# Optimization experiments

Hardware: AMD Instinct MI355X
Metric: run time of the kernel (lower is better)

Reference implementation:

```python
import jax, jax.numpy as jnp
import numpy as np

D_MODEL = 768
N_HEADS = 12
D_K = D_MODEL // N_HEADS
BATCH = 1
SEQ = 4096


def setup_inputs() -> dict:
    key = jax.random.key(0)
    kx, kq, kk, kv, ko = jax.random.split(key, 5)
    s = 1.0 / np.sqrt(D_MODEL)
    return {
        "x": jax.random.normal(kx, (BATCH, SEQ, D_MODEL), dtype=jnp.float32),
        "wq": jax.random.normal(kq, (D_MODEL, D_MODEL), dtype=jnp.float32) * s,
        "wk": jax.random.normal(kk, (D_MODEL, D_MODEL), dtype=jnp.float32) * s,
        "wv": jax.random.normal(kv, (D_MODEL, D_MODEL), dtype=jnp.float32) * s,
        "wo": jax.random.normal(ko, (D_MODEL, D_MODEL), dtype=jnp.float32) * s,
    }


def reference(x, wq, wk, wv, wo):
    B, S, D = x.shape
    H, dk = N_HEADS, D_K
    # nn.Linear(x) = x @ W.T ; reshape to [B,H,S,dk]
    def proj(w):
        return (x @ w.T).reshape(B, S, H, dk).transpose(0, 2, 1, 3)
    q, k, v = proj(wq), proj(wk), proj(wv)
    scores = jnp.einsum('bhqd,bhkd->bhqk', q, k) / np.sqrt(dk).astype(np.float32)
    attn = jax.nn.softmax(scores, axis=-1)
    out = jnp.einsum('bhqk,bhkd->bhqd', attn, v)
    out = out.transpose(0, 2, 1, 3).reshape(B, S, D)
    return out @ wo.T
```

## Files before the change

### kernel.cpp

```cpp
#include <hip/hip_runtime.h>
#include <stdint.h>

#define SEQ 4096
#define DMODEL 768
#define NHEADS 12
#define DKH 64

typedef __attribute__((ext_vector_type(8))) short short8;
typedef __attribute__((ext_vector_type(4))) float floatx4;
typedef __attribute__((ext_vector_type(16))) float floatx16;

__device__ __forceinline__ unsigned short f2bf(float f) {
    unsigned int u = __float_as_uint(f);
    u += 0x7fffu + ((u >> 16) & 1u);
    return (unsigned short)(u >> 16);
}

__device__ __forceinline__ float exp2fast(float x) {
    return __builtin_amdgcn_exp2f(x);
}

__device__ __forceinline__ unsigned int cvt_pk_bf16(float lo, float hi) {
    unsigned int r;
    asm("v_cvt_pk_bf16_f32 %0, %1, %2" : "=v"(r) : "v"(lo), "v"(hi));
    return r;
}

__device__ __forceinline__ int swz(int row, int colb) {
    return colb ^ ((row & 7) << 4);
}

__device__ __forceinline__ void async_copy16(void* lds, const void* g) {
    __builtin_amdgcn_global_load_lds(
        (const __attribute__((address_space(1))) void*)g,
        (__attribute__((address_space(3))) void*)lds,
        16, 0, 0);
}

__global__ __launch_bounds__(256) void castk(const float* __restrict__ src,
                                             unsigned short* __restrict__ dst,
                                             int n4) {
    int i = blockIdx.x * 256 + threadIdx.x;
    if (i >= n4) return;
    float4 v = ((const float4*)src)[i];
    ushort4 o;
    o.x = f2bf(v.x); o.y = f2bf(v.y); o.z = f2bf(v.z); o.w = f2bf(v.w);
    ((ushort4*)dst)[i] = o;
}

__global__ __launch_bounds__(256) void castw(const float* __restrict__ w0,
                                             const float* __restrict__ w1,
                                             const float* __restrict__ w2,
                                             const float* __restrict__ w3,
                                             unsigned short* __restrict__ dst) {
    int b = blockIdx.x;
    int wsel = b / 576;
    int i = (b % 576) * 256 + threadIdx.x;
    const float* src = (wsel == 0) ? w0 : (wsel == 1) ? w1 : (wsel == 2) ? w2 : w3;
    float4 v = ((const float4*)src)[i];
    ushort4 o;
    o.x = f2bf(v.x); o.y = f2bf(v.y); o.z = f2bf(v.z); o.w = f2bf(v.w);
    ((ushort4*)(dst + (size_t)wsel * 589824))[i] = o;
}

#define STAGE_G(bsel, kb)                                                              \
    do {                                                                               \
        char* As_ = smem + (bsel) * 24576;                                             \
        _Pragma("unroll") for (int ii = 0; ii < 4; ii++) {                             \
            int o = ii * 4096 + t * 16;                                                \
            int row = o >> 7, colb = o & 127;                                          \
            async_copy16(As_ + ii * 4096 + wid * 1024,                                 \
                         (const char*)A + ((size_t)(rowBase + row) * DMODEL + (kb)) * 2 \
                             + swz(row, colb));                                        \
        }                                                                              \
        _Pragma("unroll") for (int ii = 0; ii < 2; ii++) {                             \
            int o = ii * 4096 + t * 16;                                                \
            int row = o >> 7, colb = o & 127;                                          \
            async_copy16(As_ + 16384 + ii * 4096 + wid * 1024,                         \
                         (const char*)B + ((size_t)(colBase + row) * DMODEL + (kb)) * 2 \
                             + swz(row, colb));                                        \
        }                                                                              \
    } while (0)

#define GEMM_COMPUTE(As, Bs)                                                           \
    do {                                                                               \
        short8 a_[4][2], b_[2][2];                                                     \
        _Pragma("unroll") for (int m = 0; m < 4; m++)                                  \
            _Pragma("unroll") for (int kk = 0; kk < 2; kk++) {                         \
                int row = wr * 64 + m * 16 + lr;                                       \
                int colb = kk * 64 + lg * 16;                                          \
                a_[m][kk] = *(const short8*)((As) + row * 128 + swz(row, colb));       \
            }                                                                          \
        _Pragma("unroll") for (int n = 0; n < 2; n++)                                  \
            _Pragma("unroll") for (int kk = 0; kk < 2; kk++) {                         \
                int row = wc * 32 + n * 16 + lr;                                       \
                int colb = kk * 64 + lg * 16;                                          \
                b_[n][kk] = *(const short8*)((Bs) + row * 128 + swz(row, colb));       \
            }                                                                          \
        _Pragma("unroll") for (int m = 0; m < 4; m++)                                  \
            _Pragma("unroll") for (int n = 0; n < 2; n++)                              \
                _Pragma("unroll") for (int kk = 0; kk < 2; kk++)                       \
                    acc[m][n] = __builtin_amdgcn_mfma_f32_16x16x32_bf16(               \
                        a_[m][kk], b_[n][kk], acc[m][n], 0, 0, 0);                     \
    } while (0)

__global__ __launch_bounds__(256, 2)
void gemm_qkv(const unsigned short* __restrict__ A,
              const unsigned short* __restrict__ W,
              unsigned short* __restrict__ OutBase, float qscale) {
    __shared__ __align__(128) char smem[49152];

    const int t = threadIdx.x;
    const int wid = t >> 6, lane = t & 63;
    const int lr = lane & 15, lg = lane >> 4;
    const int wr = wid >> 1, wc = wid & 1;
    const int rowBase = blockIdx.x * 128;
    const int proj = blockIdx.y / 12;
    const int colBase = (blockIdx.y % 12) * 64;
    const unsigned short* B = W + (size_t)proj * 589824;

    const floatx4 zero4 = {0.f, 0.f, 0.f, 0.f};
    floatx4 acc[4][2];
#pragma unroll
    for (int m = 0; m < 4; m++)
#pragma unroll
        for (int n = 0; n < 2; n++) acc[m][n] = zero4;

    STAGE_G(0, 0);
    for (int i = 0; i < 12; ++i) {
        __builtin_amdgcn_s_barrier();
        __builtin_amdgcn_sched_barrier(0);
        if (i < 11) {
            STAGE_G((i + 1) & 1, (i + 1) * 64);
            asm volatile("s_waitcnt vmcnt(6)" ::: "memory");
        } else {
            asm volatile("s_waitcnt vmcnt(0)" ::: "memory");
        }
        __builtin_amdgcn_s_barrier();
        __builtin_amdgcn_sched_barrier(0);
        char* As = smem + (i & 1) * 24576;
        GEMM_COMPUTE(As, As + 16384);
    }

    if (proj < 2) {
        unsigned short* O = OutBase + (size_t)proj * 3145728;
        float scale = (proj == 0) ? qscale : 1.0f;
#pragma unroll
        for (int m = 0; m < 4; m++)
#pragma unroll
            for (int n = 0; n < 2; n++)
#pragma unroll
                for (int r = 0; r < 4; r++) {
                    int srow = rowBase + wr * 64 + m * 16 + lg * 4 + r;
                    int col = colBase + wc * 32 + n * 16 + lr;
                    int h = col >> 6, d = col & 63;
                    O[((size_t)h * SEQ + srow) * DKH + d] = f2bf(acc[m][n][r] * scale);
                }
    } else {
        unsigned short* O = OutBase + 6291456;
#pragma unroll
        for (int m = 0; m < 4; m++)
#pragma unroll
            for (int n = 0; n < 2; n++) {
                int srow0 = rowBase + wr * 64 + m * 16 + lg * 4;
                int pos0 = (srow0 & ~15) | ((srow0 & 4) << 1) | ((srow0 & 8) >> 1);
                int col = colBase + wc * 32 + n * 16 + lr;
                ushort4 o4;
                o4.x = f2bf(acc[m][n][0]);
                o4.y = f2bf(acc[m][n][1]);
                o4.z = f2bf(acc[m][n][2]);
                o4.w = f2bf(acc[m][n][3]);
                *(ushort4*)(O + (size_t)col * SEQ + pos0) = o4;
            }
    }
}

__global__ __launch_bounds__(256, 2)
void gemm_o(const unsigned short* __restrict__ A,
            const unsigned short* __restrict__ B,
            float* __restrict__ Out) {
    __shared__ __align__(128) char smem[49152];

    const int t = threadIdx.x;
    const int wid = t >> 6, lane = t & 63;
    const int lr = lane & 15, lg = lane >> 4;
    const int wr = wid >> 1, wc = wid & 1;
    const int rowBase = blockIdx.x * 128;
    const int colBase = blockIdx.y * 64;

    const floatx4 zero4 = {0.f, 0.f, 0.f, 0.f};
    floatx4 acc[4][2];
#pragma unroll
    for (int m = 0; m < 4; m++)
#pragma unroll
        for (int n = 0; n < 2; n++) acc[m][n] = zero4;

    STAGE_G(0, 0);
    for (int i = 0; i < 12; ++i) {
        __builtin_amdgcn_s_barrier();
        __builtin_amdgcn_sched_barrier(0);
        if (i < 11) {
            STAGE_G((i + 1) & 1, (i + 1) * 64);
            asm volatile("s_waitcnt vmcnt(6)" ::: "memory");
        } else {
            asm volatile("s_waitcnt vmcnt(0)" ::: "memory");
        }
        __builtin_amdgcn_s_barrier();
        __builtin_amdgcn_sched_barrier(0);
        char* As = smem + (i & 1) * 24576;
        GEMM_COMPUTE(As, As + 16384);
    }

#pragma unroll
    for (int m = 0; m < 4; m++)
#pragma unroll
        for (int n = 0; n < 2; n++)
#pragma unroll
            for (int r = 0; r < 4; r++) {
                int srow = rowBase + wr * 64 + m * 16 + lg * 4 + r;
                int col = colBase + wc * 32 + n * 16 + lr;
                Out[(size_t)srow * DMODEL + col] = acc[m][n][r];
            }
}

#define STAGE_K8(bsel, kv0)                                                            \
    do {                                                                               \
        char* Kd_ = smem + (bsel) * 16384;                                             \
        _Pragma("unroll") for (int ii = 0; ii < 4; ii++) {                             \
            int cc = ii * 256 + wid * 64 + lane;                                       \
            int gk = cc >> 6, qd = (cc >> 1) & 31, hh = cc & 1;                        \
            int kb2 = gk >> 2, ks2 = gk & 3;                                           \
            int key = kb2 * 32 + qd;                                                   \
            async_copy16(Kd_ + (ii * 256 + wid * 64) * 16,                             \
                         (const char*)(Kp + headOff) + (size_t)((kv0) + key) * 128     \
                             + (ks2 * 2 + hh) * 16);                                   \
        }                                                                              \
    } while (0)

#define STAGE_V8(kv0)                                                                  \
    do {                                                                               \
        char* Vd_ = smem + 32768;                                                      \
        _Pragma("unroll") for (int ii = 0; ii < 4; ii++) {                             \
            int cc = ii * 256 + wid * 64 + lane;                                       \
            int gv = cc >> 6, qd = (cc >> 1) & 31, hh = cc & 1;                        \
            int fbv = gv & 1, cv = (gv >> 1) & 3, ev = gv >> 3;                        \
            int feat = fbv * 32 + qd;                                                  \
            int p0 = ev * 64 + cv * 16 + hh * 8;                                       \
            async_copy16(Vd_ + (ii * 256 + wid * 64) * 16,                             \
                         (const char*)Vt                                               \
                             + ((size_t)(h * DKH + feat) * SEQ + (kv0) + p0) * 2);     \
        }                                                                              \
    } while (0)

__global__ __launch_bounds__(256, 3)
void attn_k(const unsigned short* __restrict__ Q,
            const unsigned short* __restrict__ Kp,
            const unsigned short* __restrict__ Vt,
            unsigned short* __restrict__ AO) {
    __shared__ __align__(128) char smem[49152];

    const int t = threadIdx.x;
    const int wid = t >> 6, lane = t & 63;
    const int q31 = lane & 31, hi = lane >> 5;
    const int g = wid >> 1, e = wid & 1;

    int nid = (blockIdx.x & 7) * 96 + (blockIdx.x >> 3);
    const int h = nid >> 6, qb = nid & 63;
    const size_t headOff = (size_t)h * SEQ * DKH;

    const unsigned short* qptr =
        Q + headOff + (size_t)(qb * 64 + g * 32 + q31) * DKH + hi * 8;
    short8 qf[4];
#pragma unroll
    for (int ks = 0; ks < 4; ks++) qf[ks] = *(const short8*)(qptr + ks * 16);

    const floatx16 z16 = {0.f, 0.f, 0.f, 0.f, 0.f, 0.f, 0.f, 0.f,
                          0.f, 0.f, 0.f, 0.f, 0.f, 0.f, 0.f, 0.f};
    float mrun = -3.0e38f, lrun = 0.f;
    floatx16 accO[2] = {z16, z16};

    STAGE_K8(0, 0);

    for (int tt = 0; tt < 32; ++tt) {
        asm volatile("s_waitcnt vmcnt(0)" ::: "memory");
        __builtin_amdgcn_s_barrier();
        __builtin_amdgcn_sched_barrier(0);
        STAGE_V8(tt * 128);
        if (tt < 31) STAGE_K8((tt + 1) & 1, (tt + 1) * 128);
        __builtin_amdgcn_sched_barrier(0);

        const char* Ks = smem + (tt & 1) * 16384;
        const char* Vs = smem + 32768;

        floatx16 s[2] = {z16, z16};
        __builtin_amdgcn_s_setprio(1);
#pragma unroll
        for (int kb = 0; kb < 2; kb++) {
            const int kb2 = e * 2 + kb;
#pragma unroll
            for (int ks = 0; ks < 4; ks++) {
                short8 kf = *(const short8*)(
                    Ks + ((kb2 * 4 + ks) * 64 + q31 * 2 + hi) * 16);
                s[kb] = __builtin_amdgcn_mfma_f32_32x32x16_bf16(kf, qf[ks], s[kb], 0, 0, 0);
            }
        }
        __builtin_amdgcn_s_setprio(0);

        float mk[2];
#pragma unroll
        for (int kb = 0; kb < 2; kb++) {
            float a = fmaxf(fmaxf(s[kb][0], s[kb][1]), fmaxf(s[kb][2], s[kb][3]));
            float b = fmaxf(fmaxf(s[kb][4], s[kb][5]), fmaxf(s[kb][6], s[kb][7]));
            float c = fmaxf(fmaxf(s[kb][8], s[kb][9]), fmaxf(s[kb][10], s[kb][11]));
            float d = fmaxf(fmaxf(s[kb][12], s[kb][13]), fmaxf(s[kb][14], s[kb][15]));
            mk[kb] = fmaxf(fmaxf(a, b), fmaxf(c, d));
        }
        float mt = fmaxf(mk[0], mk[1]);
        mt = fmaxf(mt, __shfl_xor(mt, 32));
        if (!__all(mt <= mrun + 8.0f)) {
            float mnew = fmaxf(mrun, mt);
            float al = exp2fast(mrun - mnew);
#pragma unroll
            for (int fb = 0; fb < 2; fb++)
#pragma unroll
                for (int j = 0; j < 16; j++) accO[fb][j] *= al;
            lrun *= al;
            mrun = mnew;
        }
#pragma unroll
        for (int kb = 0; kb < 2; kb++)
#pragma unroll
            for (int j = 0; j < 16; j++) s[kb][j] = exp2fast(s[kb][j] - mrun);
        float sum = 0.f;
#pragma unroll
        for (int kb = 0; kb < 2; kb++) {
            float a = (s[kb][0] + s[kb][1]) + (s[kb][2] + s[kb][3]);
            float b = (s[kb][4] + s[kb][5]) + (s[kb][6] + s[kb][7]);
            float c = (s[kb][8] + s[kb][9]) + (s[kb][10] + s[kb][11]);
            float d = (s[kb][12] + s[kb][13]) + (s[kb][14] + s[kb][15]);
            sum += (a + b) + (c + d);
        }
        sum += __shfl_xor(sum, 32);
        lrun += sum;

        if (tt < 31) asm volatile("s_waitcnt vmcnt(4)" ::: "memory");
        else         asm volatile("s_waitcnt vmcnt(0)" ::: "memory");
        __builtin_amdgcn_s_barrier();
        __builtin_amdgcn_sched_barrier(0);

        __builtin_amdgcn_s_setprio(1);
#pragma unroll
        for (int c = 0; c < 4; c++) {
            const int kb = c >> 1, r0 = (c & 1) * 8;
            uint4 pw;
            pw.x = cvt_pk_bf16(s[kb][r0 + 0], s[kb][r0 + 1]);
            pw.y = cvt_pk_bf16(s[kb][r0 + 2], s[kb][r0 + 3]);
            pw.z = cvt_pk_bf16(s[kb][r0 + 4], s[kb][r0 + 5]);
            pw.w = cvt_pk_bf16(s[kb][r0 + 6], s[kb][r0 + 7]);
            short8 pf = *(const short8*)&pw;
#pragma unroll
            for (int fb = 0; fb < 2; fb++) {
                short8 vf = *(const short8*)(
                    Vs + (((e * 4 + c) * 2 + fb) * 64 + q31 * 2 + hi) * 16);
                accO[fb] = __builtin_amdgcn_mfma_f32_32x32x16_bf16(vf, pf, accO[fb], 0, 0, 0);
            }
        }
        __builtin_amdgcn_s_setprio(0);
    }

    __builtin_amdgcn_s_barrier();
    char* R = smem + g * 9216 + lane * 144;
    if (e == 1) {
#pragma unroll
        for (int fb = 0; fb < 2; fb++)
#pragma unroll
            for (int j4 = 0; j4 < 4; j4++) {
                floatx4 v4 = {accO[fb][j4 * 4 + 0], accO[fb][j4 * 4 + 1],
                              accO[fb][j4 * 4 + 2], accO[fb][j4 * 4 + 3]};
                *(floatx4*)(R + fb * 64 + j4 * 16) = v4;
            }
        *(float*)(R + 128) = mrun;
        *(float*)(R + 132) = lrun;
        asm volatile("s_waitcnt lgkmcnt(0)" ::: "memory");
    }
    __builtin_amdgcn_s_barrier();
    __builtin_amdgcn_sched_barrier(0);
    if (e == 0) {
        float m1 = *(const float*)(R + 128);
        float l1 = *(const float*)(R + 132);
        float m = fmaxf(mrun, m1);
        float a0 = exp2fast(mrun - m), a1 = exp2fast(m1 - m);
        float inv = 1.0f / (lrun * a0 + l1 * a1);
        int srow = qb * 64 + g * 32 + q31;
#pragma unroll
        for (int fb = 0; fb < 2; fb++)
#pragma unroll
            for (int rq = 0; rq < 4; rq++) {
                floatx4 p4 = *(const floatx4*)(R + fb * 64 + rq * 16);
                ushort4 o4;
                o4.x = f2bf((accO[fb][4 * rq + 0] * a0 + p4[0] * a1) * inv);
                o4.y = f2bf((accO[fb][4 * rq + 1] * a0 + p4[1] * a1) * inv);
                o4.z = f2bf((accO[fb][4 * rq + 2] * a0 + p4[2] * a1) * inv);
                o4.w = f2bf((accO[fb][4 * rq + 3] * a0 + p4[3] * a1) * inv);
                int col = h * DKH + fb * 32 + rq * 8 + hi * 4;
                *(ushort4*)(AO + (size_t)srow * DMODEL + col) = o4;
            }
    }
}

extern "C" void kernel_launch(void* const* d_in, const int* in_sizes, int n_in,
                              void* d_out, int out_size, void* d_ws, size_t ws_size,
                              hipStream_t stream) {
    const float* x  = (const float*)d_in[0];
    const float* wq = (const float*)d_in[1];
    const float* wk = (const float*)d_in[2];
    const float* wv = (const float*)d_in[3];
    const float* wo = (const float*)d_in[4];

    char* ws = (char*)d_ws;
    unsigned short* xb  = (unsigned short*)(ws + 0);
    unsigned short* wqb = (unsigned short*)(ws + 6291456);
    unsigned short* wob = (unsigned short*)(ws + 9830400);
    unsigned short* Qb  = (unsigned short*)(ws + 11010048);
    unsigned short* Kb  = (unsigned short*)(ws + 17301504);
    unsigned short* VTb = (unsigned short*)(ws + 23592960);
    unsigned short* AOb = (unsigned short*)(ws + 29884416);

    castk<<<3072, 256, 0, stream>>>(x, xb, 786432);
    castw<<<2304, 256, 0, stream>>>(wq, wk, wv, wo, wqb);

    gemm_qkv<<<dim3(32, 36), 256, 0, stream>>>(xb, wqb, Qb, 0.18033688f);

    attn_k<<<dim3(768), 256, 0, stream>>>(Qb, Kb, VTb, AOb);

    gemm_o<<<dim3(32, 12), 256, 0, stream>>>(AOb, wob, (float*)d_out);
}
```

Baseline: 119.5 us.

## Process two 32-row query tiles per warp to reuse K/V fragments

Each warp now handles 64 query rows, as two 32-row sub-tiles with separate softmax state, so block query tiles grow from 64 to 128 and the grid halves to 384 blocks. Each K and V fragment read from LDS feeds two MFMAs, halving LDS traffic and global K/V staging per query. In exchange register pressure roughly doubles (launch bounds lowered to 2 blocks per SM) and there are fewer blocks, which may leave CUs underused on a 256-CU part. The epilogue scratch layout is adapted to hold both sub-tiles.

```diff
diff --git a/kernel.cpp b/kernel.cpp
--- a/kernel.cpp
+++ b/kernel.cpp
@@ -252,7 +252,7 @@
         }                                                                              \
     } while (0)
 
-__global__ __launch_bounds__(256, 3)
+__global__ __launch_bounds__(256, 2)
 void attn_k(const unsigned short* __restrict__ Q,
             const unsigned short* __restrict__ Kp,
             const unsigned short* __restrict__ Vt,
@@ -264,20 +264,26 @@
     const int q31 = lane & 31, hi = lane >> 5;
     const int g = wid >> 1, e = wid & 1;
 
-    int nid = (blockIdx.x & 7) * 96 + (blockIdx.x >> 3);
-    const int h = nid >> 6, qb = nid & 63;
+    int nid = (blockIdx.x & 7) * 48 + (blockIdx.x >> 3);
+    const int h = nid >> 5, qb = nid & 31;
     const size_t headOff = (size_t)h * SEQ * DKH;
 
-    const unsigned short* qptr =
-        Q + headOff + (size_t)(qb * 64 + g * 32 + q31) * DKH + hi * 8;
-    short8 qf[4];
-#pragma unroll
-    for (int ks = 0; ks < 4; ks++) qf[ks] = *(const short8*)(qptr + ks * 16);
+    short8 qf0[4], qf1[4];
+    {
+        const unsigned short* qp0 =
+            Q + headOff + (size_t)(qb * 128 + g * 64 + q31) * DKH + hi * 8;
+        const unsigned short* qp1 = qp0 + 32 * DKH;
+#pragma unroll
+        for (int ks = 0; ks < 4; ks++) {
+            qf0[ks] = *(const short8*)(qp0 + ks * 16);
+            qf1[ks] = *(const short8*)(qp1 + ks * 16);
+        }
+    }
 
     const floatx16 z16 = {0.f, 0.f, 0.f, 0.f, 0.f, 0.f, 0.f, 0.f,
                           0.f, 0.f, 0.f, 0.f, 0.f, 0.f, 0.f, 0.f};
-    float mrun = -3.0e38f, lrun = 0.f;
-    floatx16 accO[2] = {z16, z16};
+    float mrun[2] = {-3.0e38f, -3.0e38f}, lrun[2] = {0.f, 0.f};
+    floatx16 accO[2][2] = {{z16, z16}, {z16, z16}};
 
     STAGE_K8(0, 0);
 
@@ -292,7 +298,7 @@
         const char* Ks = smem + (tt & 1) * 16384;
         const char* Vs = smem + 32768;
 
-        floatx16 s[2] = {z16, z16};
+        floatx16 s[2][2] = {{z16, z16}, {z16, z16}};
         __builtin_amdgcn_s_setprio(1);
 #pragma unroll
         for (int kb = 0; kb < 2; kb++) {
@@ -301,47 +307,51 @@
             for (int ks = 0; ks < 4; ks++) {
                 short8 kf = *(const short8*)(
                     Ks + ((kb2 * 4 + ks) * 64 + q31 * 2 + hi) * 16);
-                s[kb] = __builtin_amdgcn_mfma_f32_32x32x16_bf16(kf, qf[ks], s[kb], 0, 0, 0);
+                s[0][kb] = __builtin_amdgcn_mfma_f32_32x32x16_bf16(kf, qf0[ks], s[0][kb], 0, 0, 0);
+                s[1][kb] = __builtin_amdgcn_mfma_f32_32x32x16_bf16(kf, qf1[ks], s[1][kb], 0, 0, 0);
             }
         }
         __builtin_amdgcn_s_setprio(0);
 
-        float mk[2];
-#pragma unroll
-        for (int kb = 0; kb < 2; kb++) {
-            float a = fmaxf(fmaxf(s[kb][0], s[kb][1]), fmaxf(s[kb][2], s[kb][3]));
-            float b = fmaxf(fmaxf(s[kb][4], s[kb][5]), fmaxf(s[kb][6], s[kb][7]));
-            float c = fmaxf(fmaxf(s[kb][8], s[kb][9]), fmaxf(s[kb][10], s[kb][11]));
-            float d = fmaxf(fmaxf(s[kb][12], s[kb][13]), fmaxf(s[kb][14], s[kb][15]));
-            mk[kb] = fmaxf(fmaxf(a, b), fmaxf(c, d));
-        }
-        float mt = fmaxf(mk[0], mk[1]);
-        mt = fmaxf(mt, __shfl_xor(mt, 32));
-        if (!__all(mt <= mrun + 8.0f)) {
-            float mnew = fmaxf(mrun, mt);
-            float al = exp2fast(mrun - mnew);
-#pragma unroll
-            for (int fb = 0; fb < 2; fb++)
-#pragma unroll
-                for (int j = 0; j < 16; j++) accO[fb][j] *= al;
-            lrun *= al;
-            mrun = mnew;
-        }
-#pragma unroll
-        for (int kb = 0; kb < 2; kb++)
-#pragma unroll
-            for (int j = 0; j < 16; j++) s[kb][j] = exp2fast(s[kb][j] - mrun);
-        float sum = 0.f;
-#pragma unroll
-        for (int kb = 0; kb < 2; kb++) {
-            float a = (s[kb][0] + s[kb][1]) + (s[kb][2] + s[kb][3]);
-            float b = (s[kb][4] + s[kb][5]) + (s[kb][6] + s[kb][7]);
-            float c = (s[kb][8] + s[kb][9]) + (s[kb][10] + s[kb][11]);
-            float d = (s[kb][12] + s[kb][13]) + (s[kb][14] + s[kb][15]);
-            sum += (a + b) + (c + d);
-        }
-        sum += __shfl_xor(sum, 32);
-        lrun += sum;
+#pragma unroll
+        for (int u = 0; u < 2; u++) {
+            float mk[2];
+#pragma unroll
+            for (int kb = 0; kb < 2; kb++) {
+                float a = fmaxf(fmaxf(s[u][kb][0], s[u][kb][1]), fmaxf(s[u][kb][2], s[u][kb][3]));
+                float b = fmaxf(fmaxf(s[u][kb][4], s[u][kb][5]), fmaxf(s[u][kb][6], s[u][kb][7]));
+                float c = fmaxf(fmaxf(s[u][kb][8], s[u][kb][9]), fmaxf(s[u][kb][10], s[u][kb][11]));
+                float d = fmaxf(fmaxf(s[u][kb][12], s[u][kb][13]), fmaxf(s[u][kb][14], s[u][kb][15]));
+                mk[kb] = fmaxf(fmaxf(a, b), fmaxf(c, d));
+            }
+            float mt = fmaxf(mk[0], mk[1]);
+            mt = fmaxf(mt, __shfl_xor(mt, 32));
+            if (!__all(mt <= mrun[u] + 8.0f)) {
+                float mnew = fmaxf(mrun[u], mt);
+                float al = exp2fast(mrun[u] - mnew);
+#pragma unroll
+                for (int fb = 0; fb < 2; fb++)
+#pragma unroll
+                    for (int j = 0; j < 16; j++) accO[u][fb][j] *= al;
+                lrun[u] *= al;
+                mrun[u] = mnew;
+            }
+#pragma unroll
+            for (int kb = 0; kb < 2; kb++)
+#pragma unroll
+                for (int j = 0; j < 16; j++) s[u][kb][j] = exp2fast(s[u][kb][j] - mrun[u]);
+            float sum = 0.f;
+#pragma unroll
+            for (int kb = 0; kb < 2; kb++) {
+                float a = (s[u][kb][0] + s[u][kb][1]) + (s[u][kb][2] + s[u][kb][3]);
+                float b = (s[u][kb][4] + s[u][kb][5]) + (s[u][kb][6] + s[u][kb][7]);
+                float c = (s[u][kb][8] + s[u][kb][9]) + (s[u][kb][10] + s[u][kb][11]);
+                float d = (s[u][kb][12] + s[u][kb][13]) + (s[u][kb][14] + s[u][kb][15]);
+                sum += (a + b) + (c + d);
+            }
+            sum += __shfl_xor(sum, 32);
+            lrun[u] += sum;
+        }
 
         if (tt < 31) asm volatile("s_waitcnt vmcnt(4)" ::: "memory");
         else         asm volatile("s_waitcnt vmcnt(0)" ::: "memory");
@@ -352,59 +362,72 @@
 #pragma unroll
         for (int c = 0; c < 4; c++) {
             const int kb = c >> 1, r0 = (c & 1) * 8;
-            uint4 pw;
-            pw.x = cvt_pk_bf16(s[kb][r0 + 0], s[kb][r0 + 1]);
-            pw.y = cvt_pk_bf16(s[kb][r0 + 2], s[kb][r0 + 3]);
-            pw.z = cvt_pk_bf16(s[kb][r0 + 4], s[kb][r0 + 5]);
-            pw.w = cvt_pk_bf16(s[kb][r0 + 6], s[kb][r0 + 7]);
-            short8 pf = *(const short8*)&pw;
+            uint4 pw0, pw1;
+            pw0.x = cvt_pk_bf16(s[0][kb][r0 + 0], s[0][kb][r0 + 1]);
+            pw0.y = cvt_pk_bf16(s[0][kb][r0 + 2], s[0][kb][r0 + 3]);
+            pw0.z = cvt_pk_bf16(s[0][kb][r0 + 4], s[0][kb][r0 + 5]);
+            pw0.w = cvt_pk_bf16(s[0][kb][r0 + 6], s[0][kb][r0 + 7]);
+            pw1.x = cvt_pk_bf16(s[1][kb][r0 + 0], s[1][kb][r0 + 1]);
+            pw1.y = cvt_pk_bf16(s[1][kb][r0 + 2], s[1][kb][r0 + 3]);
+            pw1.z = cvt_pk_bf16(s[1][kb][r0 + 4], s[1][kb][r0 + 5]);
+            pw1.w = cvt_pk_bf16(s[1][kb][r0 + 6], s[1][kb][r0 + 7]);
+            short8 pf0 = *(const short8*)&pw0;
+            short8 pf1 = *(const short8*)&pw1;
 #pragma unroll
             for (int fb = 0; fb < 2; fb++) {
                 short8 vf = *(const short8*)(
                     Vs + (((e * 4 + c) * 2 + fb) * 64 + q31 * 2 + hi) * 16);
-                accO[fb] = __builtin_amdgcn_mfma_f32_32x32x16_bf16(vf, pf, accO[fb], 0, 0, 0);
+                accO[0][fb] = __builtin_amdgcn_mfma_f32_32x32x16_bf16(vf, pf0, accO[0][fb], 0, 0, 0);
+                accO[1][fb] = __builtin_amdgcn_mfma_f32_32x32x16_bf16(vf, pf1, accO[1][fb], 0, 0, 0);
             }
         }
         __builtin_amdgcn_s_setprio(0);
     }
 
     __builtin_amdgcn_s_barrier();
-    char* R = smem + g * 9216 + lane * 144;
     if (e == 1) {
 #pragma unroll
-        for (int fb = 0; fb < 2; fb++)
-#pragma unroll
-            for (int j4 = 0; j4 < 4; j4++) {
-                floatx4 v4 = {accO[fb][j4 * 4 + 0], accO[fb][j4 * 4 + 1],
-                              accO[fb][j4 * 4 + 2], accO[fb][j4 * 4 + 3]};
-                *(floatx4*)(R + fb * 64 + j4 * 16) = v4;
-            }
-        *(float*)(R + 128) = mrun;
-        *(float*)(R + 132) = lrun;
+        for (int u = 0; u < 2; u++) {
+            char* R = smem + (((g * 2 + u) * 64) + lane) * 144;
+#pragma unroll
+            for (int fb = 0; fb < 2; fb++)
+#pragma unroll
+                for (int j4 = 0; j4 < 4; j4++) {
+                    floatx4 v4 = {accO[u][fb][j4 * 4 + 0], accO[u][fb][j4 * 4 + 1],
+                                  accO[u][fb][j4 * 4 + 2], accO[u][fb][j4 * 4 + 3]};
+                    *(floatx4*)(R + fb * 64 + j4 * 16) = v4;
+                }
+            *(float*)(R + 128) = mrun[u];
+            *(float*)(R + 132) = lrun[u];
+        }
         asm volatile("s_waitcnt lgkmcnt(0)" ::: "memory");
     }
     __builtin_amdgcn_s_barrier();
     __builtin_amdgcn_sched_barrier(0);
     if (e == 0) {
-        float m1 = *(const float*)(R + 128);
-        float l1 = *(const float*)(R + 132);
-        float m = fmaxf(mrun, m1);
-        float a0 = exp2fast(mrun - m), a1 = exp2fast(m1 - m);
-        float inv = 1.0f / (lrun * a0 + l1 * a1);
-        int srow = qb * 64 + g * 32 + q31;
-#pragma unroll
-        for (int fb = 0; fb < 2; fb++)
-#pragma unroll
-            for (int rq = 0; rq < 4; rq++) {
-                floatx4 p4 = *(const floatx4*)(R + fb * 64 + rq * 16);
-                ushort4 o4;
-                o4.x = f2bf((accO[fb][4 * rq + 0] * a0 + p4[0] * a1) * inv);
-                o4.y = f2bf((accO[fb][4 * rq + 1] * a0 + p4[1] * a1) * inv);
-                o4.z = f2bf((accO[fb][4 * rq + 2] * a0 + p4[2] * a1) * inv);
-                o4.w = f2bf((accO[fb][4 * rq + 3] * a0 + p4[3] * a1) * inv);
-                int col = h * DKH + fb * 32 + rq * 8 + hi * 4;
-                *(ushort4*)(AO + (size_t)srow * DMODEL + col) = o4;
-            }
+#pragma unroll
+        for (int u = 0; u < 2; u++) {
+            const char* R = smem + (((g * 2 + u) * 64) + lane) * 144;
+            float m1 = *(const float*)(R + 128);
+            float l1 = *(const float*)(R + 132);
+            float m = fmaxf(mrun[u], m1);
+            float a0 = exp2fast(mrun[u] - m), a1 = exp2fast(m1 - m);
+            float inv = 1.0f / (lrun[u] * a0 + l1 * a1);
+            int srow = qb * 128 + g * 64 + u * 32 + q31;
+#pragma unroll
+            for (int fb = 0; fb < 2; fb++)
+#pragma unroll
+                for (int rq = 0; rq < 4; rq++) {
+                    floatx4 p4 = *(const floatx4*)(R + fb * 64 + rq * 16);
+                    ushort4 o4;
+                    o4.x = f2bf((accO[u][fb][4 * rq + 0] * a0 + p4[0] * a1) * inv);
+                    o4.y = f2bf((accO[u][fb][4 * rq + 1] * a0 + p4[1] * a1) * inv);
+                    o4.z = f2bf((accO[u][fb][4 * rq + 2] * a0 + p4[2] * a1) * inv);
+                    o4.w = f2bf((accO[u][fb][4 * rq + 3] * a0 + p4[3] * a1) * inv);
+                    int col = h * DKH + fb * 32 + rq * 8 + hi * 4;
+                    *(ushort4*)(AO + (size_t)srow * DMODEL + col) = o4;
+                }
+        }
     }
 }
 
@@ -431,7 +454,7 @@
 
     gemm_qkv<<<dim3(32, 36), 256, 0, stream>>>(xb, wqb, Qb, 0.18033688f);
 
-    attn_k<<<dim3(768), 256, 0, stream>>>(Qb, Kb, VTb, AOb);
+    attn_k<<<dim3(384), 256, 0, stream>>>(Qb, Kb, VTb, AOb);
 
     gemm_o<<<dim3(32, 12), 256, 0, stream>>>(AOb, wob, (float*)d_out);
 }
```

After: 127.8 us. 6.9% more time.
